# Kernel tuning notes

Measured on AMD Instinct MI355X. Metric: run time of the kernel, lower is better.

## Reference

```python
import jax, jax.numpy as jnp
import numpy as np

COS_EPS = 1e-8  # torch F.cosine_similarity eps


def setup_inputs() -> dict:
    key = jax.random.key(0)
    k1, k2 = jax.random.split(key)
    x = jax.random.normal(k1, (8192, 512), dtype=jnp.float32)
    class_logits = jax.random.normal(k2, (8192, 100), dtype=jnp.float32)
    return {"x": x, "class_logits": class_logits}


def reference(x, class_logits):
    N, D = x.shape
    C = class_logits.shape[1]

    # class_logits.clone().detach()
    logits = jax.lax.stop_gradient(class_logits)
    pred = jax.nn.softmax(logits, axis=1)
    max_logit = pred.max(axis=1)          # [N]
    max_cls = pred.argmax(axis=1)         # [N] int

    # graph(): pairwise cosine similarity = normalize rows + gram matmul
    norms = jnp.linalg.norm(x, axis=1, keepdims=True)
    xn = x / jnp.maximum(norms, COS_EPS)
    mat = xn @ xn.T                       # [N, N]

    x_agg = mat @ x + x                   # [N, D]
    x_new = jax.lax.stop_gradient(x_agg)

    # update_prototype: per-class weighted scatter-add then mean over counts
    weighted = x_new * max_logit[:, None]                     # [N, D]
    sums = jax.ops.segment_sum(weighted, max_cls, num_segments=C)      # [C, D]
    counts = jax.ops.segment_sum(jnp.ones((N,), x.dtype), max_cls, num_segments=C)  # [C]
    prototypes = jnp.where(counts[:, None] > 0,
                           sums / jnp.maximum(counts, 1.0)[:, None],
                           jnp.zeros_like(sums))              # [C, D]

    # inter_class_matrix[i, j] = prototypes[j] - prototypes[i]
    inter_class_matrix = prototypes[None, :, :] - prototypes[:, None, :]  # [C, C, D]
    return prototypes, inter_class_matrix
```

## Files before the change

kernel.cpp:

```cpp
#include <hip/hip_runtime.h>
#include <math.h>

#define N_ROWS 8192
#define D_DIM  512
#define C_CLS  100

typedef unsigned short u16;
typedef unsigned int u32;
typedef __attribute__((ext_vector_type(8))) short short8;
typedef __attribute__((ext_vector_type(4))) float floatx4;

#define WS_G      0
#define WS_GP     262144
#define WS_INV    8650752
#define WS_WV     8658944
#define WS_CLS    8667136
#define WS_CNT    8675328
#define WS_OFFS   8675456
#define WS_CUR    8675584
#define WS_ORDER  8675712
#define WS_NTH    8683904
#define WS_NTL    10781056
#define WS_XTH    12878208
#define WS_XTL    14975360

__device__ __forceinline__ void split2(float v, u16& h, u16& l) {
    unsigned u = __float_as_uint(v);
    h = (u16)(u >> 16);
    float r = v - __uint_as_float(u & 0xFFFF0000u);
    l = (u16)(__float_as_uint(r) >> 16);
}

typedef const __attribute__((address_space(1))) u32* gp32;
typedef __attribute__((address_space(3))) u32* lp32;
__device__ __forceinline__ void cp16(const u16* g, u16* l) {
    __builtin_amdgcn_global_load_lds((gp32)g, (lp32)l, 16, 0, 0);
}

__global__ void k_softmax(const float* __restrict__ logits,
                          float* __restrict__ wv, int* __restrict__ cls,
                          int* __restrict__ cnt) {
    int wave = (blockIdx.x * blockDim.x + threadIdx.x) >> 6;
    int lane = threadIdx.x & 63;
    if (wave >= N_ROWS) return;
    const float* row = logits + (size_t)wave * C_CLS;
    float v1 = row[lane];
    bool has2 = (lane + 64) < C_CLS;
    float v2 = has2 ? row[lane + 64] : -INFINITY;
    float m; int idx;
    if (v2 > v1) { m = v2; idx = lane + 64; } else { m = v1; idx = lane; }
    #pragma unroll
    for (int off = 32; off >= 1; off >>= 1) {
        float om = __shfl_down(m, off);
        int   oi = __shfl_down(idx, off);
        if (om > m || (om == m && oi < idx)) { m = om; idx = oi; }
    }
    m = __shfl(m, 0);
    idx = __shfl(idx, 0);
    float s = expf(v1 - m) + (has2 ? expf(v2 - m) : 0.0f);
    #pragma unroll
    for (int off = 32; off >= 1; off >>= 1) s += __shfl_down(s, off);
    if (lane == 0) {
        wv[wave] = 1.0f / s;
        cls[wave] = idx;
        atomicAdd(&cnt[idx], 1);
    }
}

__global__ void k_norm(const float* __restrict__ x, float* __restrict__ inv) {
    int wave = (blockIdx.x * blockDim.x + threadIdx.x) >> 6;
    int lane = threadIdx.x & 63;
    if (wave >= N_ROWS) return;
    const float* row = x + (size_t)wave * D_DIM;
    float ss = 0.f;
    #pragma unroll
    for (int j = 0; j < D_DIM; j += 64) {
        float v = row[j + lane];
        ss += v * v;
    }
    #pragma unroll
    for (int off = 32; off >= 1; off >>= 1) ss += __shfl_down(ss, off);
    if (lane == 0) inv[wave] = 1.0f / fmaxf(sqrtf(ss), 1e-8f);
}

__global__ void k_scan(const int* __restrict__ cnt, int* __restrict__ offs) {
    if (threadIdx.x == 0) {
        int acc = 0;
        for (int c = 0; c < C_CLS; ++c) { offs[c] = acc; acc += cnt[c]; }
    }
}

__global__ void k_scatter(const int* __restrict__ cls, const int* __restrict__ offs,
                          int* __restrict__ cursor, int* __restrict__ order) {
    int m = blockIdx.x * 256 + threadIdx.x;
    int c = cls[m];
    int pos = atomicAdd(&cursor[c], 1);
    order[offs[c] + pos] = m;
}

#define LDT 65
__global__ __launch_bounds__(256) void k_convert(const float* __restrict__ x,
        const float* __restrict__ inv,
        u16* __restrict__ xth, u16* __restrict__ xtl,
        u16* __restrict__ nth, u16* __restrict__ ntl) {
    __shared__ unsigned xt_p[64 * LDT];
    __shared__ unsigned nt_p[64 * LDT];
    int r0 = blockIdx.x * 64, c0 = blockIdx.y * 64;
    int t = threadIdx.x;
    int r = t >> 2, cq = t & 3;
    const float* src = x + (size_t)(r0 + r) * D_DIM + c0 + cq * 16;
    float vv[16];
    {
        float4 a = *(const float4*)(src + 0);
        float4 b = *(const float4*)(src + 4);
        float4 c = *(const float4*)(src + 8);
        float4 d = *(const float4*)(src + 12);
        vv[0]=a.x; vv[1]=a.y; vv[2]=a.z; vv[3]=a.w;
        vv[4]=b.x; vv[5]=b.y; vv[6]=b.z; vv[7]=b.w;
        vv[8]=c.x; vv[9]=c.y; vv[10]=c.z; vv[11]=c.w;
        vv[12]=d.x; vv[13]=d.y; vv[14]=d.z; vv[15]=d.w;
    }
    float iv = inv[r0 + r];
    #pragma unroll
    for (int j = 0; j < 16; ++j) {
        u16 h, l, nh, nl;
        split2(vv[j], h, l);
        split2(iv * vv[j], nh, nl);
        int cl = cq * 16 + j;
        xt_p[cl * LDT + r] = ((unsigned)h  << 16) | l;
        nt_p[cl * LDT + r] = ((unsigned)nh << 16) | nl;
    }
    __syncthreads();
    int c = t >> 2, rq = (t & 3) * 16;
    size_t tbase = (size_t)(c0 + c) * N_ROWS + r0 + rq;
    {
        uint oh[8], ol[8];
        #pragma unroll
        for (int p = 0; p < 8; ++p) {
            unsigned d0 = xt_p[c * LDT + rq + 2*p];
            unsigned d1 = xt_p[c * LDT + rq + 2*p + 1];
            oh[p] = (d0 >> 16) | (d1 & 0xFFFF0000u);
            ol[p] = (d0 & 0xFFFFu) | (d1 << 16);
        }
        *(uint4*)&xth[tbase]     = make_uint4(oh[0], oh[1], oh[2], oh[3]);
        *(uint4*)&xth[tbase + 8] = make_uint4(oh[4], oh[5], oh[6], oh[7]);
        *(uint4*)&xtl[tbase]     = make_uint4(ol[0], ol[1], ol[2], ol[3]);
        *(uint4*)&xtl[tbase + 8] = make_uint4(ol[4], ol[5], ol[6], ol[7]);
    }
    {
        uint oh[8], ol[8];
        #pragma unroll
        for (int p = 0; p < 8; ++p) {
            unsigned d0 = nt_p[c * LDT + rq + 2*p];
            unsigned d1 = nt_p[c * LDT + rq + 2*p + 1];
            oh[p] = (d0 >> 16) | (d1 & 0xFFFF0000u);
            ol[p] = (d0 & 0xFFFFu) | (d1 << 16);
        }
        *(uint4*)&nth[tbase]     = make_uint4(oh[0], oh[1], oh[2], oh[3]);
        *(uint4*)&nth[tbase + 8] = make_uint4(oh[4], oh[5], oh[6], oh[7]);
        *(uint4*)&ntl[tbase]     = make_uint4(ol[0], ol[1], ol[2], ol[3]);
        *(uint4*)&ntl[tbase + 8] = make_uint4(ol[4], ol[5], ol[6], ol[7]);
    }
}

__global__ __launch_bounds__(256, 2) void k_gemm1(const u16* __restrict__ nth,
        const u16* __restrict__ ntl, const u16* __restrict__ xth,
        const u16* __restrict__ xtl, float* __restrict__ Gp) {
    __shared__ __attribute__((aligned(16))) u16 Ah[128*32], Al[128*32];
    __shared__ __attribute__((aligned(16))) u16 Bh[128*32], Bl[128*32];
    int i0 = (blockIdx.x & 3) << 7, j0 = (blockIdx.x >> 2) << 7;
    int kb = blockIdx.y << 8;
    int t = threadIdx.x, w = t >> 6, l = t & 63;
    int srow = t >> 2, scol = (t & 3) << 3;
    int lm = l & 15, lg = l >> 4;
    floatx4 acc[4][4];
    #pragma unroll
    for (int mi = 0; mi < 4; ++mi)
        #pragma unroll
        for (int ni = 0; ni < 4; ++ni) acc[mi][ni] = (floatx4){0.f,0.f,0.f,0.f};
    int d0 = srow * 32 + scol;
    int d1 = (64 + srow) * 32 + scol;
    const size_t ga0 = (size_t)(i0 + srow) * N_ROWS + kb + scol;
    const size_t ga1 = (size_t)(i0 + 64 + srow) * N_ROWS + kb + scol;
    const size_t gb0 = (size_t)(j0 + srow) * N_ROWS + kb + scol;
    const size_t gb1 = (size_t)(j0 + 64 + srow) * N_ROWS + kb + scol;
    for (int s = 0; s < 8; ++s) {
        int ks = s << 5;
        cp16(nth + ga0 + ks, Ah + d0);
        cp16(nth + ga1 + ks, Ah + d1);
        cp16(ntl + ga0 + ks, Al + d0);
        cp16(ntl + ga1 + ks, Al + d1);
        cp16(xth + gb0 + ks, Bh + d0);
        cp16(xth + gb1 + ks, Bh + d1);
        cp16(xtl + gb0 + ks, Bl + d0);
        cp16(xtl + gb1 + ks, Bl + d1);
        __syncthreads();
        short8 ah[4], al[4], bh[4], bl[4];
        #pragma unroll
        for (int mi = 0; mi < 4; ++mi) {
            int off = (((w & 1) << 6) + (mi << 4) + lm) * 32 + (lg << 3);
            ah[mi] = *(const short8*)&Ah[off];
            al[mi] = *(const short8*)&Al[off];
        }
        #pragma unroll
        for (int ni = 0; ni < 4; ++ni) {
            int off = (((w >> 1) << 6) + (ni << 4) + lm) * 32 + (lg << 3);
            bh[ni] = *(const short8*)&Bh[off];
            bl[ni] = *(const short8*)&Bl[off];
        }
        #pragma unroll
        for (int mi = 0; mi < 4; ++mi)
            #pragma unroll
            for (int ni = 0; ni < 4; ++ni) {
                acc[mi][ni] = __builtin_amdgcn_mfma_f32_16x16x32_bf16(ah[mi], bh[ni], acc[mi][ni], 0, 0, 0);
                acc[mi][ni] = __builtin_amdgcn_mfma_f32_16x16x32_bf16(ah[mi], bl[ni], acc[mi][ni], 0, 0, 0);
                acc[mi][ni] = __builtin_amdgcn_mfma_f32_16x16x32_bf16(al[mi], bh[ni], acc[mi][ni], 0, 0, 0);
            }
        __syncthreads();
    }
    float* Gb = Gp + ((size_t)blockIdx.y << 18);
    #pragma unroll
    for (int mi = 0; mi < 4; ++mi) {
        int row0 = i0 + ((w & 1) << 6) + (mi << 4) + (lg << 2);
        #pragma unroll
        for (int ni = 0; ni < 4; ++ni) {
            int col = j0 + ((w >> 1) << 6) + (ni << 4) + lm;
            #pragma unroll
            for (int r = 0; r < 4; ++r)
                Gb[(size_t)(row0 + r) * D_DIM + col] = acc[mi][ni][r];
        }
    }
}

__global__ void k_reduceG(const float* __restrict__ Gp, float* __restrict__ G) {
    int i = blockIdx.x * 256 + threadIdx.x;
    float s = 0.f;
    #pragma unroll
    for (int p = 0; p < 32; ++p) s += Gp[(size_t)p * (D_DIM * D_DIM) + i];
    G[i] = s;
}

__global__ __launch_bounds__(256) void k_protos(const float* __restrict__ x,
        const float* __restrict__ inv, const float* __restrict__ wv,
        const int* __restrict__ order, const int* __restrict__ offs,
        const int* __restrict__ cnt, const float* __restrict__ G,
        float* __restrict__ out) {
    __shared__ float u_s[D_DIM];
    int c = blockIdx.x;
    int t = threadIdx.x;
    int n = cnt[c], o = offs[c];
    float u0 = 0.f, u1 = 0.f, v0 = 0.f, v1 = 0.f;
    for (int p = 0; p < n; ++p) {
        int m = order[o + p];
        float wm = wv[m];
        float wi = wm * inv[m];
        float xa = x[(size_t)m * D_DIM + t];
        float xb = x[(size_t)m * D_DIM + t + 256];
        u0 += wi * xa; u1 += wi * xb;
        v0 += wm * xa; v1 += wm * xb;
    }
    u_s[t] = u0; u_s[t + 256] = u1;
    __syncthreads();
    float a0 = v0, a1 = v1;
    for (int k = 0; k < D_DIM; ++k) {
        float uk = u_s[k];
        const float* Gr = G + (size_t)k * D_DIM;
        a0 += uk * Gr[t];
        a1 += uk * Gr[t + 256];
    }
    float s = (n > 0) ? 1.0f / (float)n : 0.0f;
    out[(size_t)c * D_DIM + t]       = a0 * s;
    out[(size_t)c * D_DIM + t + 256] = a1 * s;
}

__global__ void k_inter(const float* __restrict__ proto, float* __restrict__ out) {
    int pair = blockIdx.x;
    int i = pair / C_CLS;
    int j = pair - i * C_CLS;
    int d = threadIdx.x << 2;
    float4 pj = *(const float4*)&proto[j * D_DIM + d];
    float4 pi = *(const float4*)&proto[i * D_DIM + d];
    float4 r;
    r.x = pj.x - pi.x; r.y = pj.y - pi.y; r.z = pj.z - pi.z; r.w = pj.w - pi.w;
    *(float4*)&out[(size_t)pair * D_DIM + d] = r;
}

extern "C" void kernel_launch(void* const* d_in, const int* in_sizes, int n_in,
                              void* d_out, int out_size, void* d_ws, size_t ws_size,
                              hipStream_t stream) {
    const float* x      = (const float*)d_in[0];
    const float* logits = (const float*)d_in[1];
    float* out = (float*)d_out;
    float* ws  = (float*)d_ws;
    float* G     = ws + WS_G;
    float* Gp    = ws + WS_GP;
    float* inv   = ws + WS_INV;
    float* wv    = ws + WS_WV;
    int*   cls   = (int*)(ws + WS_CLS);
    int*   cnt   = (int*)(ws + WS_CNT);
    int*   offs  = (int*)(ws + WS_OFFS);
    int*   cur   = (int*)(ws + WS_CUR);
    int*   order = (int*)(ws + WS_ORDER);
    u16* nth = (u16*)(ws + WS_NTH);
    u16* ntl = (u16*)(ws + WS_NTL);
    u16* xth = (u16*)(ws + WS_XTH);
    u16* xtl = (u16*)(ws + WS_XTL);

    hipMemsetAsync((void*)cnt, 0, 384 * sizeof(int), stream);
    k_softmax<<<N_ROWS / 4, 256, 0, stream>>>(logits, wv, cls, cnt);
    k_norm<<<N_ROWS / 4, 256, 0, stream>>>(x, inv);
    k_scan<<<1, 64, 0, stream>>>(cnt, offs);
    k_scatter<<<N_ROWS / 256, 256, 0, stream>>>(cls, offs, cur, order);
    k_convert<<<dim3(128, 8), 256, 0, stream>>>(x, inv, xth, xtl, nth, ntl);
    k_gemm1<<<dim3(16, 32), 256, 0, stream>>>(nth, ntl, xth, xtl, Gp);
    k_reduceG<<<D_DIM * D_DIM / 256, 256, 0, stream>>>(Gp, G);
    k_protos<<<C_CLS, 256, 0, stream>>>(x, inv, wv, order, offs, cnt, G, out);
    k_inter<<<C_CLS * C_CLS, 128, 0, stream>>>(out, out + C_CLS * D_DIM);
}
```

Baseline: 206.0 us.

## Split prototype kernel into parallel per-class accumulation and G projection

```diff
diff --git a/kernel.cpp b/kernel.cpp
--- a/kernel.cpp
+++ b/kernel.cpp
@@ -23,6 +23,8 @@
 #define WS_NTL    10781056
 #define WS_XTH    12878208
 #define WS_XTL    14975360
+#define WS_U      17072512
+#define WS_V      17123712
 
 __device__ __forceinline__ void split2(float v, u16& h, u16& l) {
     unsigned u = __float_as_uint(v);
@@ -84,10 +86,19 @@
 }
 
 __global__ void k_scan(const int* __restrict__ cnt, int* __restrict__ offs) {
-    if (threadIdx.x == 0) {
-        int acc = 0;
-        for (int c = 0; c < C_CLS; ++c) { offs[c] = acc; acc += cnt[c]; }
-    }
+    __shared__ int s[128];
+    int t = threadIdx.x;
+    int v = (t < C_CLS) ? cnt[t] : 0;
+    s[t] = v;
+    __syncthreads();
+    #pragma unroll
+    for (int d = 1; d < 128; d <<= 1) {
+        int add = (t >= d) ? s[t - d] : 0;
+        __syncthreads();
+        s[t] += add;
+        __syncthreads();
+    }
+    if (t < C_CLS) offs[t] = s[t] - v;
 }
 
 __global__ void k_scatter(const int* __restrict__ cls, const int* __restrict__ offs,
@@ -240,37 +251,49 @@
     G[i] = s;
 }
 
-__global__ __launch_bounds__(256) void k_protos(const float* __restrict__ x,
+__global__ __launch_bounds__(256) void k_uv(const float* __restrict__ x,
         const float* __restrict__ inv, const float* __restrict__ wv,
         const int* __restrict__ order, const int* __restrict__ offs,
-        const int* __restrict__ cnt, const float* __restrict__ G,
-        float* __restrict__ out) {
-    __shared__ float u_s[D_DIM];
-    int c = blockIdx.x;
-    int t = threadIdx.x;
+        const int* __restrict__ cnt, float* __restrict__ u, float* __restrict__ v) {
+    __shared__ float us[4][64], vs[4][64];
+    int c = blockIdx.x, jc = blockIdx.y;
+    int t = threadIdx.x, g = t >> 6, lane = t & 63;
+    int j = jc * 64 + lane;
     int n = cnt[c], o = offs[c];
-    float u0 = 0.f, u1 = 0.f, v0 = 0.f, v1 = 0.f;
-    for (int p = 0; p < n; ++p) {
+    float ua = 0.f, va = 0.f;
+    for (int p = g; p < n; p += 4) {
         int m = order[o + p];
         float wm = wv[m];
         float wi = wm * inv[m];
-        float xa = x[(size_t)m * D_DIM + t];
-        float xb = x[(size_t)m * D_DIM + t + 256];
-        u0 += wi * xa; u1 += wi * xb;
-        v0 += wm * xa; v1 += wm * xb;
-    }
-    u_s[t] = u0; u_s[t + 256] = u1;
+        float xv = x[(size_t)m * D_DIM + j];
+        ua += wi * xv; va += wm * xv;
+    }
+    us[g][lane] = ua; vs[g][lane] = va;
     __syncthreads();
-    float a0 = v0, a1 = v1;
-    for (int k = 0; k < D_DIM; ++k) {
-        float uk = u_s[k];
-        const float* Gr = G + (size_t)k * D_DIM;
-        a0 += uk * Gr[t];
-        a1 += uk * Gr[t + 256];
-    }
+    if (g == 0) {
+        float uu = us[0][lane] + us[1][lane] + us[2][lane] + us[3][lane];
+        float vv2 = vs[0][lane] + vs[1][lane] + vs[2][lane] + vs[3][lane];
+        u[(size_t)c * D_DIM + j] = uu;
+        v[(size_t)c * D_DIM + j] = vv2;
+    }
+}
+
+__global__ __launch_bounds__(256) void k_pgemm(const float* __restrict__ u,
+        const float* __restrict__ v, const int* __restrict__ cnt,
+        const float* __restrict__ G, float* __restrict__ out) {
+    __shared__ float us[D_DIM];
+    int c = blockIdx.x >> 1;
+    int j = ((blockIdx.x & 1) << 8) + threadIdx.x;
+    us[threadIdx.x]       = u[(size_t)c * D_DIM + threadIdx.x];
+    us[threadIdx.x + 256] = u[(size_t)c * D_DIM + threadIdx.x + 256];
+    __syncthreads();
+    float acc = v[(size_t)c * D_DIM + j];
+    #pragma unroll 8
+    for (int k = 0; k < D_DIM; ++k)
+        acc += us[k] * G[(size_t)k * D_DIM + j];
+    int n = cnt[c];
     float s = (n > 0) ? 1.0f / (float)n : 0.0f;
-    out[(size_t)c * D_DIM + t]       = a0 * s;
-    out[(size_t)c * D_DIM + t + 256] = a1 * s;
+    out[(size_t)c * D_DIM + j] = acc * s;
 }
 
 __global__ void k_inter(const float* __restrict__ proto, float* __restrict__ out) {
@@ -305,15 +328,18 @@
     u16* ntl = (u16*)(ws + WS_NTL);
     u16* xth = (u16*)(ws + WS_XTH);
     u16* xtl = (u16*)(ws + WS_XTL);
+    float* u_arr = ws + WS_U;
+    float* v_arr = ws + WS_V;
 
     hipMemsetAsync((void*)cnt, 0, 384 * sizeof(int), stream);
     k_softmax<<<N_ROWS / 4, 256, 0, stream>>>(logits, wv, cls, cnt);
     k_norm<<<N_ROWS / 4, 256, 0, stream>>>(x, inv);
-    k_scan<<<1, 64, 0, stream>>>(cnt, offs);
+    k_scan<<<1, 128, 0, stream>>>(cnt, offs);
     k_scatter<<<N_ROWS / 256, 256, 0, stream>>>(cls, offs, cur, order);
     k_convert<<<dim3(128, 8), 256, 0, stream>>>(x, inv, xth, xtl, nth, ntl);
     k_gemm1<<<dim3(16, 32), 256, 0, stream>>>(nth, ntl, xth, xtl, Gp);
     k_reduceG<<<D_DIM * D_DIM / 256, 256, 0, stream>>>(Gp, G);
-    k_protos<<<C_CLS, 256, 0, stream>>>(x, inv, wv, order, offs, cnt, G, out);
+    k_uv<<<dim3(C_CLS, 8), 256, 0, stream>>>(x, inv, wv, order, offs, cnt, u_arr, v_arr);
+    k_pgemm<<<C_CLS * 2, 256, 0, stream>>>(u_arr, v_arr, cnt, G, out);
     k_inter<<<C_CLS * C_CLS, 128, 0, stream>>>(out, out + C_CLS * D_DIM);
 }
```

Measured after the change: 199.9 us. 1.03x faster.
